# Performance work log

Hardware: AMD Instinct MI355X
Metric: run time of the kernel (lower is better)

The kernel has to match this reference:

```python
import jax, jax.numpy as jnp
import numpy as np

LN_EPS = 1e-5
DIM = 128
HEADS = 6
DIM_HEAD = 32
INNER = HEADS * DIM_HEAD          # 192
FF_INNER = int(DIM * 4 * 2 / 3)   # 341 (GEGLU inner dim)
LOCAL_WINDOW = 200
CACHE = 3
COMPRESS = 2
TW = LOCAL_WINDOW + CACHE         # 203
B = 2
T = 12800                         # 32 chunks of 400


def layer_norm(x, w, b):
    m = x.mean(-1, keepdims=True)
    v = ((x - m) ** 2).mean(-1, keepdims=True)
    return (x - m) / jnp.sqrt(v + LN_EPS) * w + b


def apply_rotary(q, k):
    # q, k: (b, h, n, d); standard half-rotation rotary over absolute positions
    d = q.shape[-1]
    n = q.shape[2]
    inv_freq = 1.0 / (10000.0 ** (jnp.arange(0, d, 2, dtype=jnp.float32) / d))
    freqs = jnp.arange(n, dtype=jnp.float32)[:, None] * inv_freq  # (n, d/2)
    emb = jnp.concatenate([freqs, freqs], axis=-1)                # (n, d)
    cos = jnp.cos(emb).astype(q.dtype)
    sin = jnp.sin(emb).astype(q.dtype)

    def rot_half(x):
        x1, x2 = jnp.split(x, 2, axis=-1)
        return jnp.concatenate([-x2, x1], axis=-1)

    rope = lambda x: x * cos + rot_half(x) * sin
    return rope(q), rope(k)


def local_attention(q, k, v, w):
    # causal local attention, look_backward=1 window, look_forward=0 (lucidrains LocalAttention)
    b, h, n, d = q.shape
    nw = n // w
    q, k = apply_rotary(q, k)
    qw = q.reshape(b, h, nw, w, d)

    def look_around(x):
        xw = x.reshape(b, h, nw, w, d)
        prev = jnp.pad(xw[:, :, :-1], ((0, 0), (0, 0), (1, 0), (0, 0), (0, 0)))
        return jnp.concatenate([prev, xw], axis=3)  # (b,h,nw,2w,d)

    kw = look_around(k)
    vw = look_around(v)

    t = jnp.arange(n).reshape(nw, w)
    tk_prev = jnp.pad(t[:-1], ((1, 0), (0, 0)), constant_values=-1)
    tk = jnp.concatenate([tk_prev, t], axis=1)  # (nw, 2w); -1 marks padding
    mask = (t[:, :, None] >= tk[:, None, :]) & (tk[:, None, :] >= 0)  # (nw, w, 2w)

    sim = jnp.einsum('bhwid,bhwjd->bhwij', qw, kw) * (d ** -0.5)
    neg = jnp.finfo(sim.dtype).min
    sim = jnp.where(mask[None, None], sim, neg)
    attn = jax.nn.softmax(sim, axis=-1)
    out = jnp.einsum('bhwij,bhwjd->bhwid', attn, vw)
    return out.reshape(b, h, n, d)


def local_mha(x, ln_w, ln_b, wqkv, wo, window):
    h = layer_norm(x, ln_w, ln_b)
    qkv = h @ wqkv                       # (b, n, 3*INNER)
    q, k, v = jnp.split(qkv, 3, axis=-1)

    def split_heads(t):
        bb, n, _ = t.shape
        return t.reshape(bb, n, HEADS, DIM_HEAD).transpose(0, 2, 1, 3)

    out = local_attention(split_heads(q), split_heads(k), split_heads(v), window)
    bb, hh, n, d = out.shape
    out = out.transpose(0, 2, 1, 3).reshape(bb, n, hh * d)
    return out @ wo


def feed_forward(x, ln_w, ln_b, w1, w2):
    h = layer_norm(x, ln_w, ln_b) @ w1   # (b, n, 2*FF_INNER)
    a, gate = jnp.split(h, 2, axis=-1)
    return (a * jax.nn.gelu(gate, approximate=False)) @ w2


def local_trans(x, ln1_w, ln1_b, wqkv, wo, ln2_w, ln2_b, w1, w2, window):
    n_layers = ln1_w.shape[0]
    for i in range(n_layers):
        x = x + local_mha(x, ln1_w[i], ln1_b[i], wqkv[i], wo[i], window)
        x = x + feed_forward(x, ln2_w[i], ln2_b[i], w1[i], w2[i])
    return x


def setup_inputs() -> dict:
    key = jax.random.key(0)
    ks = jax.random.split(key, 16)
    std = 0.02
    rn = lambda k, shape: jax.random.normal(k, shape, dtype=jnp.float32) * std
    inp = {
        'x': jax.random.normal(ks[0], (B, DIM, T), dtype=jnp.float32),
        'cache_token': jax.random.normal(ks[1], (1, CACHE * COMPRESS, DIM), dtype=jnp.float32),
    }
    ki = 2
    for g in ('dt', 'lt'):
        inp[g + '_ln1_w'] = jnp.ones((2, DIM), jnp.float32)
        inp[g + '_ln1_b'] = jnp.zeros((2, DIM), jnp.float32)
        inp[g + '_wqkv'] = rn(ks[ki], (2, DIM, 3 * INNER)); ki += 1
        inp[g + '_wo'] = rn(ks[ki], (2, INNER, DIM)); ki += 1
        inp[g + '_ln2_w'] = jnp.ones((2, DIM), jnp.float32)
        inp[g + '_ln2_b'] = jnp.zeros((2, DIM), jnp.float32)
        inp[g + '_w1'] = rn(ks[ki], (2, DIM, 2 * FF_INNER)); ki += 1
        inp[g + '_w2'] = rn(ks[ki], (2, FF_INNER, DIM)); ki += 1
    inp['conv_w'] = rn(ks[ki], (DIM, DIM, COMPRESS)); ki += 1
    inp['conv_b'] = jnp.zeros((DIM,), jnp.float32)
    return inp


def reference(x, cache_token,
              dt_ln1_w, dt_ln1_b, dt_wqkv, dt_wo, dt_ln2_w, dt_ln2_b, dt_w1, dt_w2,
              lt_ln1_w, lt_ln1_b, lt_wqkv, lt_wo, lt_ln2_w, lt_ln2_b, lt_w1, lt_w2,
              conv_w, conv_b):
    feat = x.transpose(0, 2, 1)                     # (B, T, C)
    b, t, c = feat.shape
    chunk = LOCAL_WINDOW * COMPRESS                 # 400
    nchunks = t // chunk
    feat = feat.reshape(b, nchunks, chunk, c)
    ct = jnp.broadcast_to(cache_token[:, None], (b, nchunks, CACHE * COMPRESS, c))
    feat = jnp.concatenate([ct, feat], axis=2)      # interleave cache tokens per chunk
    feat = feat.reshape(b, nchunks * (chunk + CACHE * COMPRESS), c)

    # DownTrans: 2-layer local transformer (window 406) + strided conv compress
    feat = local_trans(feat, dt_ln1_w, dt_ln1_b, dt_wqkv, dt_wo,
                       dt_ln2_w, dt_ln2_b, dt_w1, dt_w2, TW * COMPRESS)
    y = jax.lax.conv_general_dilated(
        feat.transpose(0, 2, 1), conv_w, (COMPRESS,), 'VALID',
        dimension_numbers=('NCH', 'OIH', 'NCH')) + conv_b[None, :, None]
    feat = y.transpose(0, 2, 1)                     # (B, n/2, C)

    # remaining depth-2 local transformer (window 203)
    feat = local_trans(feat, lt_ln1_w, lt_ln1_b, lt_wqkv, lt_wo,
                       lt_ln2_w, lt_ln2_b, lt_w1, lt_w2, TW)
    return feat
```

## Files before the change

### kernel.cpp

```cpp
#include <hip/hip_runtime.h>
#include <cstdint>
#include <cstddef>

#define DIM    128
#define HEADS  6
#define INNER  192
#define QKV3   576
#define FFI    341
#define FF2    682
#define GGP    352
#define BATCH  2
#define T_IN   12800
#define N1     12992
#define N2     6496
#define ROWS1  (BATCH * N1)
#define ROWS2  (BATCH * N2)
#define W_DT   406
#define W_LT   203

typedef unsigned short ushortT;
typedef unsigned int u32;
typedef __bf16 bf16x8 __attribute__((ext_vector_type(8)));
typedef float f32x4 __attribute__((ext_vector_type(4)));

__device__ __forceinline__ f32x4 mfma16(bf16x8 a, bf16x8 b, f32x4 c) {
  return __builtin_amdgcn_mfma_f32_16x16x32_bf16(a, b, c, 0, 0, 0);
}
__device__ __forceinline__ ushortT f2bf(float x) {
  union { __bf16 b; ushortT u; } c; c.b = (__bf16)x; return c.u;
}
__device__ __forceinline__ void async_copy16(const ushortT* g, ushortT* l) {
  __builtin_amdgcn_global_load_lds(
      (const __attribute__((address_space(1))) unsigned int*)g,
      (__attribute__((address_space(3))) unsigned int*)l, 16, 0, 0);
}

static constexpr size_t OF_FEAT = 0;
static constexpr size_t OF_H    = OF_FEAT + (size_t)ROWS1 * DIM;
static constexpr size_t OF_QKH  = OF_H + (size_t)ROWS1 * DIM / 2;
static constexpr size_t SZ_QKH  = ((size_t)(ROWS1 + 128) * 384) / 2;
static constexpr size_t OF_AO   = OF_QKH + SZ_QKH;
static constexpr size_t OF_VT   = OF_AO + (size_t)ROWS1 * INNER / 2;
static constexpr size_t SZ_VT   = ((size_t)384 * (N1 + 128)) / 2;
static constexpr size_t OF_GG   = OF_VT + SZ_VT;
static constexpr size_t OF_F2   = OF_GG + (size_t)ROWS1 * GGP / 2;
static constexpr size_t OF_WT   = OF_F2 + (size_t)ROWS2 * DIM;
static constexpr size_t WT_QKV = 0;
static constexpr size_t WT_WO  = 81920;
static constexpr size_t WT_W1  = 106496;
static constexpr size_t WT_W2  = 204800;
static constexpr size_t WT_SET = 249856;
static constexpr size_t OF_CW  = OF_WT + (4 * WT_SET) / 2 + 64;
static constexpr size_t OF_ROPE = OF_CW + (128 * 256) / 2 + 64;
static constexpr size_t OF_H2  = OF_ROPE + (size_t)N1 * 32;

__global__ void build_feat_kernel(const float* __restrict__ x,
                                  const float* __restrict__ cache,
                                  float* __restrict__ feat) {
  int idx = blockIdx.x * 256 + threadIdx.x;
  if (idx >= ROWS1 * DIM) return;
  int d = idx & 127;
  int row = idx >> 7;
  int b = row / N1;
  int i = row - b * N1;
  int c = i / 406;
  int j = i - c * 406;
  float v;
  if (j < 6) v = cache[j * DIM + d];
  else       v = x[((size_t)b * DIM + d) * T_IN + (c * 400 + j - 6)];
  feat[idx] = v;
}

__global__ __launch_bounds__(256) void ln_kernel(const float* __restrict__ x,
                                                 ushortT* __restrict__ y,
                                                 const float* __restrict__ w,
                                                 const float* __restrict__ bb,
                                                 int rows) {
  int row = blockIdx.x * 4 + (threadIdx.x >> 6);
  if (row >= rows) return;
  int lane = threadIdx.x & 63;
  const float* xr = x + (size_t)row * DIM;
  float2 v = *(const float2*)(xr + lane * 2);
  float s = v.x + v.y;
#pragma unroll
  for (int off = 32; off; off >>= 1) s += __shfl_xor(s, off);
  float mean = s * (1.0f / 128.0f);
  float dx = v.x - mean, dy = v.y - mean;
  float q = dx * dx + dy * dy;
#pragma unroll
  for (int off = 32; off; off >>= 1) q += __shfl_xor(q, off);
  float rstd = rsqrtf(q * (1.0f / 128.0f) + 1e-5f);
  float2 wv = *(const float2*)(w + lane * 2);
  float2 bv = *(const float2*)(bb + lane * 2);
  u32 packed = (u32)f2bf(dx * rstd * wv.x + bv.x) |
               ((u32)f2bf(dy * rstd * wv.y + bv.y) << 16);
  *(u32*)(y + (size_t)row * DIM + lane * 2) = packed;
}

__global__ __launch_bounds__(256) void gemm_nln(
    const ushortT* __restrict__ A, int lda,
    const ushortT* __restrict__ Wt, int ldw,
    const float* __restrict__ C, float* __restrict__ Co,
    const float* __restrict__ bias,
    int M, int Kpad, int addC,
    const float* __restrict__ lnw, const float* __restrict__ lnb,
    ushortT* __restrict__ hout, ushortT* __restrict__ bfout) {
  __shared__ ushortT As[64 * 32];
  __shared__ ushortT Bs[128 * 32];
  __shared__ float lnS[64][4];
  const int tid = threadIdx.x;
  const int wid = tid >> 6, lane = tid & 63;
  const int ck = lane & 15, quad = lane >> 4;
  const int bm = blockIdx.y * 64;
  const int wr = (wid >> 1) * 32, wc = (wid & 1) * 64;
  const int half = wid & 1;
  f32x4 acc[2][4];
#pragma unroll
  for (int t = 0; t < 2; t++)
#pragma unroll
    for (int u = 0; u < 4; u++) acc[t][u] = (f32x4){0.f, 0.f, 0.f, 0.f};

  for (int k0 = 0; k0 < Kpad; k0 += 32) {
    __syncthreads();
    {
      int idx = wid * 64 + lane;
      int row = idx >> 2, seg = (idx & 3) << 3;
      async_copy16(A + (size_t)(bm + row) * lda + k0 + seg, As + (size_t)(wid * 64) * 8);
    }
#pragma unroll
    for (int c2 = 0; c2 < 2; c2++) {
      int idx = c2 * 256 + wid * 64 + lane;
      int row = idx >> 2, seg = (idx & 3) << 3;
      async_copy16(Wt + (size_t)row * ldw + k0 + seg, Bs + (size_t)(c2 * 256 + wid * 64) * 8);
    }
    __syncthreads();
    bf16x8 af[2], bfr[4];
#pragma unroll
    for (int t = 0; t < 2; t++)
      af[t] = *(const bf16x8*)&As[(wr + t * 16 + ck) * 32 + quad * 8];
#pragma unroll
    for (int u = 0; u < 4; u++)
      bfr[u] = *(const bf16x8*)&Bs[(wc + u * 16 + ck) * 32 + quad * 8];
#pragma unroll
    for (int t = 0; t < 2; t++)
#pragma unroll
      for (int u = 0; u < 4; u++)
        acc[t][u] = mfma16(af[t], bfr[u], acc[t][u]);
  }

  float bv4[4] = {0.f, 0.f, 0.f, 0.f};
  if (bias) {
#pragma unroll
    for (int u = 0; u < 4; u++) bv4[u] = bias[wc + u * 16 + ck];
  }
  float res[2][4][4];
#pragma unroll
  for (int t = 0; t < 2; t++) {
#pragma unroll
    for (int r = 0; r < 4; r++) {
      int row = bm + wr + t * 16 + quad * 4 + r;
      const float* crow = C + (size_t)row * DIM;
#pragma unroll
      for (int u = 0; u < 4; u++) {
        int col = wc + u * 16 + ck;
        float v = acc[t][u][r] + bv4[u];
        if (addC) v += crow[col];
        res[t][r][u] = v;
      }
      if (Co) {
        float* orow = Co + (size_t)row * DIM;
#pragma unroll
        for (int u = 0; u < 4; u++) orow[wc + u * 16 + ck] = res[t][r][u];
      }
      if (bfout) {
        ushortT* brow = bfout + (size_t)row * DIM;
#pragma unroll
        for (int u = 0; u < 4; u++) brow[wc + u * 16 + ck] = f2bf(res[t][r][u]);
      }
    }
  }

  if (hout) {
#pragma unroll
    for (int t = 0; t < 2; t++) {
#pragma unroll
      for (int r = 0; r < 4; r++) {
        float s1 = ((res[t][r][0] + res[t][r][1]) + (res[t][r][2] + res[t][r][3]));
        float s2 = ((res[t][r][0] * res[t][r][0] + res[t][r][1] * res[t][r][1]) +
                    (res[t][r][2] * res[t][r][2] + res[t][r][3] * res[t][r][3]));
        s1 += __shfl_xor(s1, 1); s2 += __shfl_xor(s2, 1);
        s1 += __shfl_xor(s1, 2); s2 += __shfl_xor(s2, 2);
        s1 += __shfl_xor(s1, 4); s2 += __shfl_xor(s2, 4);
        s1 += __shfl_xor(s1, 8); s2 += __shfl_xor(s2, 8);
        if (ck == 0) {
          int rowIn = wr + t * 16 + quad * 4 + r;
          lnS[rowIn][half * 2]     = s1;
          lnS[rowIn][half * 2 + 1] = s2;
        }
      }
    }
    __syncthreads();
    float lw[4], lb[4];
#pragma unroll
    for (int u = 0; u < 4; u++) {
      lw[u] = lnw[wc + u * 16 + ck];
      lb[u] = lnb[wc + u * 16 + ck];
    }
#pragma unroll
    for (int t = 0; t < 2; t++) {
#pragma unroll
      for (int r = 0; r < 4; r++) {
        int rowIn = wr + t * 16 + quad * 4 + r;
        float S1 = lnS[rowIn][0] + lnS[rowIn][2];
        float S2 = lnS[rowIn][1] + lnS[rowIn][3];
        float mean = S1 * (1.0f / 128.0f);
        float var = S2 * (1.0f / 128.0f) - mean * mean;
        float rstd = rsqrtf(var + 1e-5f);
        ushortT* hrow = hout + (size_t)(bm + rowIn) * DIM;
#pragma unroll
        for (int u = 0; u < 4; u++) {
          int col = wc + u * 16 + ck;
          hrow[col] = f2bf((res[t][r][u] - mean) * rstd * lw[u] + lb[u]);
        }
      }
    }
  }
}

__global__ __launch_bounds__(256) void gemm_qkv(
    const ushortT* __restrict__ A,
    const ushortT* __restrict__ Wt,
    const float2* __restrict__ rope,
    ushortT* __restrict__ qkh,
    ushortT* __restrict__ vt,
    int M, int nseq, int nseqP) {
  __shared__ ushortT As[128 * 32];
  __shared__ ushortT Bs[128 * 32];
  const int tid = threadIdx.x;
  const int wid = tid >> 6, lane = tid & 63;
  const int ck = lane & 15, quad = lane >> 4;
  const int bm = blockIdx.y * 128, bn = blockIdx.x * 128;
  const int wr = (wid >> 1) * 64, wc = (wid & 1) * 64;
  f32x4 acc[4][4];
#pragma unroll
  for (int t = 0; t < 4; t++)
#pragma unroll
    for (int u = 0; u < 4; u++) acc[t][u] = (f32x4){0.f, 0.f, 0.f, 0.f};

  for (int k0 = 0; k0 < 128; k0 += 32) {
    __syncthreads();
#pragma unroll
    for (int c2 = 0; c2 < 2; c2++) {
      int idx = c2 * 256 + wid * 64 + lane;
      int row = idx >> 2, seg = (idx & 3) << 3;
      int ar = bm + row; if (ar > M - 1) ar = M - 1;
      async_copy16(A + (size_t)ar * 128 + k0 + seg, As + (size_t)(c2 * 256 + wid * 64) * 8);
      async_copy16(Wt + (size_t)(bn + row) * 128 + k0 + seg, Bs + (size_t)(c2 * 256 + wid * 64) * 8);
    }
    __syncthreads();
    bf16x8 af[4], bfr[4];
#pragma unroll
    for (int t = 0; t < 4; t++)
      af[t] = *(const bf16x8*)&As[(wr + t * 16 + ck) * 32 + quad * 8];
#pragma unroll
    for (int u = 0; u < 4; u++)
      bfr[u] = *(const bf16x8*)&Bs[(wc + u * 16 + ck) * 32 + quad * 8];
#pragma unroll
    for (int t = 0; t < 4; t++)
#pragma unroll
      for (int u = 0; u < 4; u++)
        acc[t][u] = mfma16(af[t], bfr[u], acc[t][u]);
  }

  const int s = bn + wc;
  if (s >= QKV3) return;

  if (s < 384) {
    const bool isQ = s < 192;
    const float SCq = 0.17677669529663687f * 1.4426950408889634f;
#pragma unroll
    for (int t = 0; t < 4; t++) {
#pragma unroll
      for (int r = 0; r < 4; r++) {
        int row = bm + wr + t * 16 + quad * 4 + r;
        if (row >= M) continue;
        int pos = (row >= nseq) ? row - nseq : row;
        float2 cssn = rope[pos * 16 + ck];
        float cs = cssn.x, sn = cssn.y;
        ushortT* orow = qkh + (size_t)row * 384;
#pragma unroll
        for (int u = 0; u < 4; u += 2) {
          float a0 = acc[t][u][r], a1 = acc[t][u + 1][r];
          float o0 = a0 * cs - a1 * sn;
          float o1 = a1 * cs + a0 * sn;
          if (isQ) { o0 *= SCq; o1 *= SCq; }
          int c0 = s + u * 16 + ck;
          orow[c0]      = f2bf(o0);
          orow[c0 + 16] = f2bf(o1);
        }
      }
    }
  } else {
#pragma unroll
    for (int t = 0; t < 4; t++) {
      int rowb = bm + wr + t * 16 + quad * 4;
      if (rowb >= M) continue;
      int bb = (rowb >= nseq) ? 1 : 0;
      int posb = rowb - bb * nseq;
#pragma unroll
      for (int u = 0; u < 4; u++) {
        int cv = s - 384 + u * 16 + ck;
        int hh = cv >> 5, d = cv & 31;
        ushort4 o;
        o.x = f2bf(acc[t][u][0]);
        o.y = f2bf(acc[t][u][1]);
        o.z = f2bf(acc[t][u][2]);
        o.w = f2bf(acc[t][u][3]);
        *(ushort4*)(vt + ((size_t)((bb * 6 + hh) * 32 + d)) * nseqP + posb) = o;
      }
    }
  }
}

__global__ __launch_bounds__(256) void gemm_w1g(
    const ushortT* __restrict__ A,
    const ushortT* __restrict__ Wt,
    ushortT* __restrict__ gg,
    int M) {
  __shared__ ushortT As[128 * 32];
  __shared__ ushortT Bs[128 * 32];
  const int tid = threadIdx.x;
  const int wid = tid >> 6, lane = tid & 63;
  const int ck = lane & 15, quad = lane >> 4;
  const int bm = blockIdx.y * 128, bn = blockIdx.x * 128;
  const int wr = (wid >> 1) * 64, wc = (wid & 1) * 64;
  f32x4 acc[4][4];
#pragma unroll
  for (int t = 0; t < 4; t++)
#pragma unroll
    for (int u = 0; u < 4; u++) acc[t][u] = (f32x4){0.f, 0.f, 0.f, 0.f};

  for (int k0 = 0; k0 < 128; k0 += 32) {
    __syncthreads();
#pragma unroll
    for (int c2 = 0; c2 < 2; c2++) {
      int idx = c2 * 256 + wid * 64 + lane;
      int row = idx >> 2, seg = (idx & 3) << 3;
      int ar = bm + row; if (ar > M - 1) ar = M - 1;
      async_copy16(A + (size_t)ar * 128 + k0 + seg, As + (size_t)(c2 * 256 + wid * 64) * 8);
      async_copy16(Wt + (size_t)(bn + row) * 128 + k0 + seg, Bs + (size_t)(c2 * 256 + wid * 64) * 8);
    }
    __syncthreads();
    bf16x8 af[4], bfr[4];
#pragma unroll
    for (int t = 0; t < 4; t++)
      af[t] = *(const bf16x8*)&As[(wr + t * 16 + ck) * 32 + quad * 8];
#pragma unroll
    for (int u = 0; u < 4; u++)
      bfr[u] = *(const bf16x8*)&Bs[(wc + u * 16 + ck) * 32 + quad * 8];
#pragma unroll
    for (int t = 0; t < 4; t++)
#pragma unroll
      for (int u = 0; u < 4; u++)
        acc[t][u] = mfma16(af[t], bfr[u], acc[t][u]);
  }

  const int s = bn + wc;
  if (s >= 704) return;
#pragma unroll
  for (int t = 0; t < 4; t++) {
#pragma unroll
    for (int r = 0; r < 4; r++) {
      int row = bm + wr + t * 16 + quad * 4 + r;
      if (row >= M) continue;
      ushortT* orow = gg + (size_t)row * GGP;
#pragma unroll
      for (int u = 0; u < 4; u += 2) {
        float a  = acc[t][u][r];
        float gt = acc[t][u + 1][r];
        float ge = 0.5f * gt * (1.0f + erff(gt * 0.70710678118654752f));
        int p = ((s + u * 16) >> 5) * 16 + ck;
        orow[p] = f2bf(a * ge);
      }
    }
  }
}

__global__ __launch_bounds__(256) void attn_kernel(
    const ushortT* __restrict__ qkh, const ushortT* __restrict__ vt,
    ushortT* __restrict__ out, int nseq, int nseqP, int w, int nw) {
  __shared__ ushortT Ks[128 * 40];
  __shared__ ushortT Vs[32 * 136];
  __shared__ ushortT Ps[4 * 16 * 72];

  const int bx = blockIdx.x;
  const int c = bx % nw;
  const int g = bx / nw;
  const int h = blockIdx.y;
  const int b = blockIdx.z;
  const int tid = threadIdx.x;
  const int wv = tid >> 6;
  const int lane = tid & 63;
  const int ck = lane & 15;
  const int quad = lane >> 4;

  const ushortT* gq = qkh + (size_t)b * nseq * 384;
  const ushortT* gv = vt + ((size_t)(b * 6 + h) * 32) * nseqP;
  const int cw = c * w;
  const int q0 = g * 64;
  const int qt = q0 + wv * 16;
  const bool wave_on = qt < w;

  const int j0 = (c > 0) ? (c - 1) * w : 0;
  const int jend_block = cw + min(q0 + 63, w - 1) + 1;
  const int jend_wave = wave_on ? (cw + min(qt + 15, w - 1) + 1) : 0;

  bf16x8 qf;
  {
    int qrow = cw + min(qt + ck, w - 1);
    qf = *(const bf16x8*)(gq + (size_t)qrow * 384 + h * 32 + quad * 8);
  }

  f32x4 olo = {0.f, 0.f, 0.f, 0.f};
  f32x4 ohi = {0.f, 0.f, 0.f, 0.f};
  float lp[4] = {0.f, 0.f, 0.f, 0.f};
  ushortT* pw = Ps + wv * 16 * 72;

  for (int tb = j0; tb < jend_block; tb += 128) {
    __syncthreads();
    for (int i = tid; i < 512; i += 256) {
      int row = i >> 2, dg = (i & 3) << 3;
      *(float4*)&Ks[row * 40 + dg] =
          *(const float4*)(gq + (size_t)(tb + row) * 384 + 192 + h * 32 + dg);
    }
    for (int i = tid; i < 512; i += 256) {
      int d = i >> 4, kg = (i & 15) << 3;
      *(float4*)&Vs[d * 136 + kg] = *(const float4*)(gv + (size_t)d * nseqP + tb + kg);
    }
    __syncthreads();

    const int glim = min(128, jend_wave - tb);
    for (int g64 = 0; g64 < glim; g64 += 64) {
      int r0 = g64 + 2 * ck;
      bf16x8 kf0 = *(const bf16x8*)&Ks[(r0) * 40 + quad * 8];
      bf16x8 kf1 = *(const bf16x8*)&Ks[(r0 + 1) * 40 + quad * 8];
      bf16x8 kf2 = *(const bf16x8*)&Ks[(r0 + 32) * 40 + quad * 8];
      bf16x8 kf3 = *(const bf16x8*)&Ks[(r0 + 33) * 40 + quad * 8];
      f32x4 z = {0.f, 0.f, 0.f, 0.f};
      f32x4 s0 = mfma16(qf, kf0, z);
      f32x4 s1 = mfma16(qf, kf1, z);
      f32x4 s2 = mfma16(qf, kf2, z);
      f32x4 s3 = mfma16(qf, kf3, z);
      if (tb + g64 + 63 > cw + qt) {
        int key0 = tb + g64 + 2 * ck;
#pragma unroll
        for (int r = 0; r < 4; r++) {
          int qg = cw + qt + quad * 4 + r;
          if (key0 > qg)      s0[r] = -__builtin_inff();
          if (key0 + 1 > qg)  s1[r] = -__builtin_inff();
          if (key0 + 32 > qg) s2[r] = -__builtin_inff();
          if (key0 + 33 > qg) s3[r] = -__builtin_inff();
        }
      }
#pragma unroll
      for (int r = 0; r < 4; r++) {
        float p0 = exp2f(s0[r]);
        float p1 = exp2f(s1[r]);
        float p2 = exp2f(s2[r]);
        float p3 = exp2f(s3[r]);
        lp[r] += (p0 + p1) + (p2 + p3);
        int row72 = (quad * 4 + r) * 72;
        *(u32*)&pw[row72 + 2 * ck]      = (u32)f2bf(p0) | ((u32)f2bf(p1) << 16);
        *(u32*)&pw[row72 + 32 + 2 * ck] = (u32)f2bf(p2) | ((u32)f2bf(p3) << 16);
      }
      bf16x8 pf0 = *(const bf16x8*)&pw[ck * 72 + quad * 8];
      bf16x8 pf1 = *(const bf16x8*)&pw[ck * 72 + 32 + quad * 8];
      bf16x8 vlo0 = *(const bf16x8*)&Vs[ck * 136 + g64 + quad * 8];
      bf16x8 vhi0 = *(const bf16x8*)&Vs[(ck + 16) * 136 + g64 + quad * 8];
      bf16x8 vlo1 = *(const bf16x8*)&Vs[ck * 136 + g64 + 32 + quad * 8];
      bf16x8 vhi1 = *(const bf16x8*)&Vs[(ck + 16) * 136 + g64 + 32 + quad * 8];
      olo = mfma16(pf0, vlo0, olo);
      olo = mfma16(pf1, vlo1, olo);
      ohi = mfma16(pf0, vhi0, ohi);
      ohi = mfma16(pf1, vhi1, ohi);
    }
  }

  if (wave_on) {
#pragma unroll
    for (int r = 0; r < 4; r++) {
      float lr = lp[r];
      lr += __shfl_xor(lr, 1);
      lr += __shfl_xor(lr, 2);
      lr += __shfl_xor(lr, 4);
      lr += __shfl_xor(lr, 8);
      int qi = qt + quad * 4 + r;
      if (qi < w) {
        float inv = 1.0f / lr;
        ushortT* orow = out + ((size_t)b * nseq + cw + qi) * INNER + h * 32;
        orow[ck]      = f2bf(olo[r] * inv);
        orow[ck + 16] = f2bf(ohi[r] * inv);
      }
    }
  }
}

__global__ void wconvert_all_kernel(
    const float* __restrict__ dq, const float* __restrict__ dwo,
    const float* __restrict__ dw1, const float* __restrict__ dw2,
    const float* __restrict__ lq, const float* __restrict__ lwo,
    const float* __restrict__ lw1, const float* __restrict__ lw2,
    const float* __restrict__ convw,
    ushortT* __restrict__ wt, ushortT* __restrict__ cwt,
    float2* __restrict__ rope) {
  int idx = blockIdx.x * 256 + threadIdx.x;
  const int TOTW = 4 * (int)WT_SET;
  const int CWN = 128 * 256;
  if (idx < TOTW) {
    int s = idx / (int)WT_SET;
    int rem = idx - s * (int)WT_SET;
    int lyr = s & 1;
    const float* Wq = ((s < 2) ? dq : lq) + (size_t)lyr * DIM * QKV3;
    const float* Wo = ((s < 2) ? dwo : lwo) + (size_t)lyr * INNER * DIM;
    const float* W1 = ((s < 2) ? dw1 : lw1) + (size_t)lyr * DIM * FF2;
    const float* W2 = ((s < 2) ? dw2 : lw2) + (size_t)lyr * FFI * DIM;
    float v = 0.f;
    if (rem < (int)WT_WO) {
      int n = rem >> 7, k = rem & 127;
      if (n < QKV3) v = Wq[(size_t)k * QKV3 + n];
    } else if (rem < (int)WT_W1) {
      int r = rem - (int)WT_WO;
      int n = r / INNER, k = r - n * INNER;
      v = Wo[(size_t)k * DIM + n];
    } else if (rem < (int)WT_W2) {
      int r = rem - (int)WT_W1;
      int n = r >> 7, k = r & 127;
      if (n < 704) {
        int blk = n >> 5, wi = n & 31;
        int p = blk * 16 + (wi & 15);
        if (p < FFI) {
          int src = (wi < 16) ? p : FFI + p;
          v = W1[(size_t)k * FF2 + src];
        }
      }
    } else {
      int r = rem - (int)WT_W2;
      int n = r / GGP, k = r - n * GGP;
      if (k < FFI) v = W2[(size_t)k * DIM + n];
    }
    wt[idx] = f2bf(v);
  } else if (idx < TOTW + CWN) {
    int r = idx - TOTW;
    int o = r >> 8, k = r & 255;
    int kk = k >> 7, i = k & 127;
    cwt[r] = f2bf(convw[((size_t)o * DIM + i) * 2 + kk]);
  } else {
    int r = idx - TOTW - CWN;
    if (r < N1 * 16) {
      int pos = r >> 4, k = r & 15;
      float invf = 1.0f / powf(10000.0f, (float)k * (1.0f / 16.0f));
      float sn, cs;
      sincosf((float)pos * invf, &sn, &cs);
      rope[r] = make_float2(cs, sn);
    }
  }
}

static void run_layer(float* F, float* Fout, ushortT* hbuf, ushortT* qkh, ushortT* vtb,
                      ushortT* attnb, ushortT* ggb, const ushortT* wt,
                      const float2* rope,
                      int M, int nseq, int w,
                      const float* ln2w, const float* ln2b,
                      const float* nlnw, const float* nlnb,
                      ushortT* w2bf, hipStream_t stream) {
  int nseqP = nseq + 128;
  int gy = (M + 127) / 128;
  int gy64 = M / 64;
  gemm_qkv<<<dim3(5, gy), 256, 0, stream>>>(hbuf, wt + WT_QKV, rope, qkh, vtb, M, nseq, nseqP);
  int nw = nseq / w;
  int qgroups = (w + 63) / 64;
  attn_kernel<<<dim3(nw * qgroups, HEADS, BATCH), 256, 0, stream>>>(qkh, vtb, attnb,
                                                                    nseq, nseqP, w, nw);
  gemm_nln<<<dim3(1, gy64), 256, 0, stream>>>(attnb, INNER, wt + WT_WO, INNER, F, F,
                                              nullptr, M, INNER, 1, ln2w, ln2b,
                                              hbuf, nullptr);
  gemm_w1g<<<dim3(6, gy), 256, 0, stream>>>(hbuf, wt + WT_W1, ggb, M);
  gemm_nln<<<dim3(1, gy64), 256, 0, stream>>>(ggb, GGP, wt + WT_W2, GGP, F, Fout,
                                              nullptr, M, GGP, 1, nlnw, nlnb,
                                              nlnw ? hbuf : (ushortT*)nullptr, w2bf);
}

extern "C" void kernel_launch(void* const* d_in, const int* in_sizes, int n_in,
                              void* d_out, int out_size, void* d_ws, size_t ws_size,
                              hipStream_t stream) {
  const float* x        = (const float*)d_in[0];
  const float* cache    = (const float*)d_in[1];
  const float* dt_ln1_w = (const float*)d_in[2];
  const float* dt_ln1_b = (const float*)d_in[3];
  const float* dt_wqkv  = (const float*)d_in[4];
  const float* dt_wo    = (const float*)d_in[5];
  const float* dt_ln2_w = (const float*)d_in[6];
  const float* dt_ln2_b = (const float*)d_in[7];
  const float* dt_w1    = (const float*)d_in[8];
  const float* dt_w2    = (const float*)d_in[9];
  const float* lt_ln1_w = (const float*)d_in[10];
  const float* lt_ln1_b = (const float*)d_in[11];
  const float* lt_wqkv  = (const float*)d_in[12];
  const float* lt_wo    = (const float*)d_in[13];
  const float* lt_ln2_w = (const float*)d_in[14];
  const float* lt_ln2_b = (const float*)d_in[15];
  const float* lt_w1    = (const float*)d_in[16];
  const float* lt_w2    = (const float*)d_in[17];
  const float* conv_w   = (const float*)d_in[18];
  const float* conv_b   = (const float*)d_in[19];

  float* ws     = (float*)d_ws;
  float* feat   = ws + OF_FEAT;
  ushortT* h    = (ushortT*)(ws + OF_H);
  ushortT* qkh  = (ushortT*)(ws + OF_QKH);
  ushortT* attnb= (ushortT*)(ws + OF_AO);
  ushortT* vtb  = (ushortT*)(ws + OF_VT);
  ushortT* ggb  = (ushortT*)(ws + OF_GG);
  float* feat2  = ws + OF_F2;
  ushortT* wt   = (ushortT*)(ws + OF_WT);
  ushortT* cwt  = (ushortT*)(ws + OF_CW);
  float2* rope  = (float2*)(ws + OF_ROPE);
  ushortT* h2   = (ushortT*)(ws + OF_H2);
  float* outf   = (float*)d_out;

  {
    int total = 4 * (int)WT_SET + 128 * 256 + N1 * 16;
    wconvert_all_kernel<<<(total + 255) / 256, 256, 0, stream>>>(
        dt_wqkv, dt_wo, dt_w1, dt_w2, lt_wqkv, lt_wo, lt_w1, lt_w2,
        conv_w, wt, cwt, rope);
  }

  build_feat_kernel<<<(ROWS1 * DIM + 255) / 256, 256, 0, stream>>>(x, cache, feat);
  ln_kernel<<<ROWS1 / 4, 256, 0, stream>>>(feat, h, dt_ln1_w, dt_ln1_b, ROWS1);

  run_layer(feat, feat, h, qkh, vtb, attnb, ggb, wt + 0 * WT_SET, rope,
            ROWS1, N1, W_DT,
            dt_ln2_w, dt_ln2_b, dt_ln1_w + DIM, dt_ln1_b + DIM, nullptr, stream);
  run_layer(feat, nullptr, h, qkh, vtb, attnb, ggb, wt + 1 * WT_SET, rope,
            ROWS1, N1, W_DT,
            dt_ln2_w + DIM, dt_ln2_b + DIM, nullptr, nullptr, h, stream);

  gemm_nln<<<dim3(1, ROWS2 / 64), 256, 0, stream>>>(h, 256, cwt, 256,
                                                    feat2, feat2, conv_b,
                                                    ROWS2, 256, 0,
                                                    lt_ln1_w, lt_ln1_b, h2, nullptr);

  run_layer(feat2, feat2, h2, qkh, vtb, attnb, ggb, wt + 2 * WT_SET, rope,
            ROWS2, N2, W_LT,
            lt_ln2_w, lt_ln2_b, lt_ln1_w + DIM, lt_ln1_b + DIM, nullptr, stream);
  run_layer(feat2, outf, h2, qkh, vtb, attnb, ggb, wt + 3 * WT_SET, rope,
            ROWS2, N2, W_LT,
            lt_ln2_w + DIM, lt_ln2_b + DIM, nullptr, nullptr, nullptr, stream);
}
```

Before: 576.2 us.

## Pipeline attention K/V tiles through registers with XOR-swizzled 64-key LDS tiles

The attention kernel now stages K and V in 64-key tiles in place of 128-key tiles. It prefetches the next tile into registers while computing on the current one, and stores tiles in an XOR-swizzled LDS layout so fragment reads avoid bank conflicts without padding. Query groups are issued in reverse order so the heavier late groups start first, which should balance load. The smaller tile means more barriers per block, but the load latency is now hidden behind the MFMA and exp work.

```diff
diff --git a/kernel.cpp b/kernel.cpp
--- a/kernel.cpp
+++ b/kernel.cpp
@@ -388,14 +388,14 @@
 
 __global__ __launch_bounds__(256) void attn_kernel(
     const ushortT* __restrict__ qkh, const ushortT* __restrict__ vt,
-    ushortT* __restrict__ out, int nseq, int nseqP, int w, int nw) {
-  __shared__ ushortT Ks[128 * 40];
-  __shared__ ushortT Vs[32 * 136];
+    ushortT* __restrict__ out, int nseq, int nseqP, int w, int nw, int qgroups) {
+  __shared__ ushortT Ks[64 * 32];
+  __shared__ ushortT Vs[32 * 64];
   __shared__ ushortT Ps[4 * 16 * 72];
 
   const int bx = blockIdx.x;
   const int c = bx % nw;
-  const int g = bx / nw;
+  const int g = (qgroups - 1) - bx / nw;
   const int h = blockIdx.y;
   const int b = blockIdx.z;
   const int tid = threadIdx.x;
@@ -421,38 +421,44 @@
     qf = *(const bf16x8*)(gq + (size_t)qrow * 384 + h * 32 + quad * 8);
   }
 
+  const int dstSlot = tid ^ ((tid >> 3) & 7);
+  const int krow = tid >> 2, kch = tid & 3;
+  const ushortT* ksrc = gq + (size_t)krow * 384 + 192 + h * 32 + kch * 8;
+  const int vd = tid >> 3, vks = tid & 7;
+  const ushortT* vsrc = gv + (size_t)vd * nseqP + vks * 8;
+
+  const int p0 = (8 * ck + quad) ^ (ck & 7);
+  const int p1 = (8 * ck + quad + 4) ^ (ck & 7);
+
   f32x4 olo = {0.f, 0.f, 0.f, 0.f};
   f32x4 ohi = {0.f, 0.f, 0.f, 0.f};
   float lp[4] = {0.f, 0.f, 0.f, 0.f};
   ushortT* pw = Ps + wv * 16 * 72;
 
-  for (int tb = j0; tb < jend_block; tb += 128) {
-    __syncthreads();
-    for (int i = tid; i < 512; i += 256) {
-      int row = i >> 2, dg = (i & 3) << 3;
-      *(float4*)&Ks[row * 40 + dg] =
-          *(const float4*)(gq + (size_t)(tb + row) * 384 + 192 + h * 32 + dg);
-    }
-    for (int i = tid; i < 512; i += 256) {
-      int d = i >> 4, kg = (i & 15) << 3;
-      *(float4*)&Vs[d * 136 + kg] = *(const float4*)(gv + (size_t)d * nseqP + tb + kg);
-    }
-    __syncthreads();
-
-    const int glim = min(128, jend_wave - tb);
-    for (int g64 = 0; g64 < glim; g64 += 64) {
-      int r0 = g64 + 2 * ck;
-      bf16x8 kf0 = *(const bf16x8*)&Ks[(r0) * 40 + quad * 8];
-      bf16x8 kf1 = *(const bf16x8*)&Ks[(r0 + 1) * 40 + quad * 8];
-      bf16x8 kf2 = *(const bf16x8*)&Ks[(r0 + 32) * 40 + quad * 8];
-      bf16x8 kf3 = *(const bf16x8*)&Ks[(r0 + 33) * 40 + quad * 8];
+  float4 kreg = *(const float4*)(ksrc + (size_t)j0 * 384);
+  float4 vreg = *(const float4*)(vsrc + j0);
+
+  for (int tb = j0; tb < jend_block; tb += 64) {
+    __syncthreads();
+    *(float4*)&Ks[(size_t)dstSlot * 8] = kreg;
+    *(float4*)&Vs[(size_t)dstSlot * 8] = vreg;
+    __syncthreads();
+    if (tb + 64 < jend_block) {
+      kreg = *(const float4*)(ksrc + (size_t)(tb + 64) * 384);
+      vreg = *(const float4*)(vsrc + tb + 64);
+    }
+    if (tb < jend_wave) {
+      bf16x8 kf0 = *(const bf16x8*)&Ks[p0 * 8];
+      bf16x8 kf1 = *(const bf16x8*)&Ks[p1 * 8];
+      bf16x8 kf2 = *(const bf16x8*)&Ks[p0 * 8 + 1024];
+      bf16x8 kf3 = *(const bf16x8*)&Ks[p1 * 8 + 1024];
       f32x4 z = {0.f, 0.f, 0.f, 0.f};
       f32x4 s0 = mfma16(qf, kf0, z);
       f32x4 s1 = mfma16(qf, kf1, z);
       f32x4 s2 = mfma16(qf, kf2, z);
       f32x4 s3 = mfma16(qf, kf3, z);
-      if (tb + g64 + 63 > cw + qt) {
-        int key0 = tb + g64 + 2 * ck;
+      if (tb + 63 > cw + qt) {
+        int key0 = tb + 2 * ck;
 #pragma unroll
         for (int r = 0; r < 4; r++) {
           int qg = cw + qt + quad * 4 + r;
@@ -464,21 +470,21 @@
       }
 #pragma unroll
       for (int r = 0; r < 4; r++) {
-        float p0 = exp2f(s0[r]);
-        float p1 = exp2f(s1[r]);
-        float p2 = exp2f(s2[r]);
-        float p3 = exp2f(s3[r]);
-        lp[r] += (p0 + p1) + (p2 + p3);
+        float pp0 = exp2f(s0[r]);
+        float pp1 = exp2f(s1[r]);
+        float pp2 = exp2f(s2[r]);
+        float pp3 = exp2f(s3[r]);
+        lp[r] += (pp0 + pp1) + (pp2 + pp3);
         int row72 = (quad * 4 + r) * 72;
-        *(u32*)&pw[row72 + 2 * ck]      = (u32)f2bf(p0) | ((u32)f2bf(p1) << 16);
-        *(u32*)&pw[row72 + 32 + 2 * ck] = (u32)f2bf(p2) | ((u32)f2bf(p3) << 16);
+        *(u32*)&pw[row72 + 2 * ck]      = (u32)f2bf(pp0) | ((u32)f2bf(pp1) << 16);
+        *(u32*)&pw[row72 + 32 + 2 * ck] = (u32)f2bf(pp2) | ((u32)f2bf(pp3) << 16);
       }
       bf16x8 pf0 = *(const bf16x8*)&pw[ck * 72 + quad * 8];
       bf16x8 pf1 = *(const bf16x8*)&pw[ck * 72 + 32 + quad * 8];
-      bf16x8 vlo0 = *(const bf16x8*)&Vs[ck * 136 + g64 + quad * 8];
-      bf16x8 vhi0 = *(const bf16x8*)&Vs[(ck + 16) * 136 + g64 + quad * 8];
-      bf16x8 vlo1 = *(const bf16x8*)&Vs[ck * 136 + g64 + 32 + quad * 8];
-      bf16x8 vhi1 = *(const bf16x8*)&Vs[(ck + 16) * 136 + g64 + 32 + quad * 8];
+      bf16x8 vlo0 = *(const bf16x8*)&Vs[p0 * 8];
+      bf16x8 vlo1 = *(const bf16x8*)&Vs[p1 * 8];
+      bf16x8 vhi0 = *(const bf16x8*)&Vs[p0 * 8 + 1024];
+      bf16x8 vhi1 = *(const bf16x8*)&Vs[p1 * 8 + 1024];
       olo = mfma16(pf0, vlo0, olo);
       olo = mfma16(pf1, vlo1, olo);
       ohi = mfma16(pf0, vhi0, ohi);
@@ -580,7 +586,7 @@
   int nw = nseq / w;
   int qgroups = (w + 63) / 64;
   attn_kernel<<<dim3(nw * qgroups, HEADS, BATCH), 256, 0, stream>>>(qkh, vtb, attnb,
-                                                                    nseq, nseqP, w, nw);
+                                                                    nseq, nseqP, w, nw, qgroups);
   gemm_nln<<<dim3(1, gy64), 256, 0, stream>>>(attnb, INNER, wt + WT_WO, INNER, F, F,
                                               nullptr, M, INNER, 1, ln2w, ln2b,
                                               hbuf, nullptr);
```

Result: faster. 548.9 us (-4.7%).
